# Kernel optimization log

Measured on AMD Instinct MI355X. Metric: run time of the kernel, lower is better.

The kernel has to match this reference:

```python
import jax, jax.numpy as jnp
import numpy as np

N_NODES = 50000
N_EDGES = 1600000
D_IN = 128
D_HID = 128
D_OUT = 3
EPS = 1e-5


def setup_inputs() -> dict:
    key = jax.random.key(0)
    ks = jax.random.split(key, 16)
    def lin(k, fi, fo):
        s = 1.0 / np.sqrt(fi)
        return jax.random.uniform(k, (fi, fo), jnp.float32, -s, s)
    inp = {
        "x": jax.random.normal(ks[0], (N_NODES, D_IN), jnp.float32),
        "edge_index": jax.random.randint(ks[1], (2, N_EDGES), 0, N_NODES, jnp.int32),
        "W1": lin(ks[2], D_IN, D_HID), "b1": jnp.zeros((D_HID,), jnp.float32),
        "W2": lin(ks[3], D_HID, D_HID), "b2": jnp.zeros((D_HID,), jnp.float32),
        "W3": lin(ks[4], D_HID, D_HID), "b3": jnp.zeros((D_HID,), jnp.float32),
        "g1": jnp.ones((D_HID,), jnp.float32), "beta1": jnp.zeros((D_HID,), jnp.float32),
        "g2": jnp.ones((D_HID,), jnp.float32), "beta2": jnp.zeros((D_HID,), jnp.float32),
        "Wp1": lin(ks[5], D_HID, D_HID), "bp1": jnp.zeros((D_HID,), jnp.float32),
        "Wp2": lin(ks[6], D_HID, D_OUT), "bp2": jnp.zeros((D_OUT,), jnp.float32),
    }
    return inp


def _gcn_norm(edge_index, n):
    # add self-loops, symmetric normalization (PyG GCNConv default)
    loops = jnp.arange(n, dtype=edge_index.dtype)
    row = jnp.concatenate([edge_index[0], loops])  # source
    col = jnp.concatenate([edge_index[1], loops])  # target
    deg = jax.ops.segment_sum(jnp.ones_like(col, jnp.float32), col, num_segments=n)
    dinv = jnp.where(deg > 0, jax.lax.rsqrt(deg), 0.0)
    norm = dinv[row] * dinv[col]  # [E+N]
    return row, col, norm


def _gcn_conv(x, W, b, row, col, norm, n):
    h = x @ W                                # [N, F]
    msg = h[row] * norm[:, None]             # [E+N, F] gather
    out = jax.ops.segment_sum(msg, col, num_segments=n)  # scatter-add
    return out + b


def _layernorm(x, g, beta):
    mu = jnp.mean(x, axis=-1, keepdims=True)
    var = jnp.var(x, axis=-1, keepdims=True)
    return (x - mu) * jax.lax.rsqrt(var + EPS) * g + beta


def reference(x, edge_index, W1, b1, W2, b2, W3, b3, g1, beta1, g2, beta2, Wp1, bp1, Wp2, bp2):
    n = x.shape[0]
    row, col, norm = _gcn_norm(edge_index, n)
    # layer 0
    h = _gcn_conv(x, W1, b1, row, col, norm, n)
    h = _layernorm(jax.nn.relu(h), g1, beta1)  # dropout = identity (eval mode)
    # layer 1
    h = _gcn_conv(h, W2, b2, row, col, norm, n)
    h = _layernorm(jax.nn.relu(h), g2, beta2)
    # layer 2 (no layernorm)
    h = _gcn_conv(h, W3, b3, row, col, norm, n)
    h = jax.nn.relu(h)
    # post-MP MLP head (dropout = identity in eval)
    h = h @ Wp1 + bp1
    return h @ Wp2 + bp2
```

## Files before the change

kernel.cpp:

```cpp
#include <hip/hip_runtime.h>
#include <hip/hip_bf16.h>

#define EPS_LN 1e-5f
#define NB    256
#define SEGCAP 16384

typedef int ivec4 __attribute__((ext_vector_type(4)));
typedef short bf16x8v __attribute__((ext_vector_type(8)));
typedef float f32x4v __attribute__((ext_vector_type(4)));
typedef unsigned short u16x8 __attribute__((ext_vector_type(8)));


__global__ __launch_bounds__(256) void bucket_hist(const int* __restrict__ col,
                                                   int* __restrict__ chunkBH,
                                                   int E, int per, int nbuck) {
    __shared__ int hist[256];
    int t = threadIdx.x;
    hist[t] = 0;
    __syncthreads();
    int s0 = blockIdx.x * per;
    int s1 = s0 + per; if (s1 > E) s1 = E;
    if (s0 < s1) {
        int q0 = s0 >> 2, q1 = s1 >> 2;
        for (int i = q0 + t; i < q1; i += 256) {
            ivec4 c = __builtin_nontemporal_load((const ivec4*)col + i);
            atomicAdd(&hist[c.x >> 8], 1);
            atomicAdd(&hist[c.y >> 8], 1);
            atomicAdd(&hist[c.z >> 8], 1);
            atomicAdd(&hist[c.w >> 8], 1);
        }
        for (int i = (q1 << 2) + t; i < s1; i += 256)
            atomicAdd(&hist[col[i] >> 8], 1);
    }
    __syncthreads();
    if (t < nbuck) chunkBH[blockIdx.x * 256 + t] = hist[t];
}

__global__ __launch_bounds__(256) void bucket_scan(int* __restrict__ chunkBH,
                                                   int* __restrict__ bucketStart,
                                                   int* __restrict__ rowPtr,
                                                   int E, int n, int nbuck, int nb) {
    __shared__ int tot[256];
    int t = threadIdx.x;
    int run = 0;
    if (t < nbuck) {
        for (int k0 = 0; k0 < nb; k0 += 16) {
            int v[16];
#pragma unroll
            for (int j = 0; j < 16; j++)
                v[j] = (k0 + j < nb) ? chunkBH[(k0 + j) * 256 + t] : 0;
#pragma unroll
            for (int j = 0; j < 16; j++) {
                int tv = v[j];
                if (k0 + j < nb) chunkBH[(k0 + j) * 256 + t] = run;
                run += tv;
            }
        }
    }
    tot[t] = run;
    __syncthreads();
    for (int d = 1; d < 256; d <<= 1) {
        int add = (t >= d) ? tot[t - d] : 0;
        __syncthreads();
        tot[t] += add;
        __syncthreads();
    }
    if (t < nbuck) bucketStart[t] = tot[t] - run;
    if (t == 0) { bucketStart[nbuck] = E; rowPtr[n] = E; }
}

__global__ __launch_bounds__(256) void scatter_pairs(const int* __restrict__ row,
                                                     const int* __restrict__ col,
                                                     const int* __restrict__ chunkBH,
                                                     const int* __restrict__ bucketStart,
                                                     unsigned long long* __restrict__ tmp,
                                                     int E, int per, int nbuck) {
    __shared__ int curs[256];
    int t = threadIdx.x;
    int k = blockIdx.x;
    curs[t] = (t < nbuck) ? (chunkBH[k * 256 + t] + bucketStart[t]) : 0;
    __syncthreads();
    int s0 = k * per;
    int s1 = s0 + per; if (s1 > E) s1 = E;
    if (s0 >= s1) return;
    int q0 = s0 >> 2, q1 = s1 >> 2;
    for (int i = q0 + t; i < q1; i += 256) {
        ivec4 c4 = __builtin_nontemporal_load((const ivec4*)col + i);
        ivec4 r4 = __builtin_nontemporal_load((const ivec4*)row + i);
        int p0 = atomicAdd(&curs[c4.x >> 8], 1);
        tmp[p0] = ((unsigned long long)(unsigned)c4.x << 32) | (unsigned)r4.x;
        int p1 = atomicAdd(&curs[c4.y >> 8], 1);
        tmp[p1] = ((unsigned long long)(unsigned)c4.y << 32) | (unsigned)r4.y;
        int p2 = atomicAdd(&curs[c4.z >> 8], 1);
        tmp[p2] = ((unsigned long long)(unsigned)c4.z << 32) | (unsigned)r4.z;
        int p3 = atomicAdd(&curs[c4.w >> 8], 1);
        tmp[p3] = ((unsigned long long)(unsigned)c4.w << 32) | (unsigned)r4.w;
    }
    for (int i = (q1 << 2) + t; i < s1; i += 256) {
        int c = col[i], r = row[i];
        int p = atomicAdd(&curs[c >> 8], 1);
        tmp[p] = ((unsigned long long)(unsigned)c << 32) | (unsigned)r;
    }
}

__global__ __launch_bounds__(256) void bucket_fill(const unsigned long long* __restrict__ tmp,
                                                   const int* __restrict__ bucketStart,
                                                   int* __restrict__ rowPtr,
                                                   float* __restrict__ dinv,
                                                   int* __restrict__ srcList,
                                                   int n) {
    __shared__ int cnt[256];
    __shared__ int cur[256];
    __shared__ int seg[SEGCAP];
    int b = blockIdx.x, t = threadIdx.x;
    int node0 = b << 8;
    int s0 = bucketStart[b], s1 = bucketStart[b + 1];
    int len = s1 - s0;
    cnt[t] = 0;
    __syncthreads();
    for (int i = s0 + t; i < s1; i += 256) {
        int c = (int)(tmp[i] >> 32);
        atomicAdd(&cnt[c - node0], 1);
    }
    __syncthreads();
    int v = cnt[t];
    cur[t] = v;
    __syncthreads();
    for (int d = 1; d < 256; d <<= 1) {
        int add = (t >= d) ? cur[t - d] : 0;
        __syncthreads();
        cur[t] += add;
        __syncthreads();
    }
    int excl = cur[t] - v;
    int node = node0 + t;
    if (node < n) {
        rowPtr[node] = s0 + excl;
        dinv[node] = rsqrtf((float)v + 1.0f);
    }
    cur[t] = excl;
    __syncthreads();
    if (len <= SEGCAP) {
        for (int i = s0 + t; i < s1; i += 256) {
            unsigned long long p = tmp[i];
            int c = (int)(p >> 32);
            int r = (int)(p & 0xffffffffu);
            int pos = atomicAdd(&cur[c - node0], 1);
            seg[pos] = r;
        }
        __syncthreads();
        for (int i = t; i < len; i += 256)
            srcList[s0 + i] = seg[i];
    } else {
        for (int i = s0 + t; i < s1; i += 256) {
            unsigned long long p = tmp[i];
            int c = (int)(p >> 32);
            int r = (int)(p & 0xffffffffu);
            int pos = atomicAdd(&cur[c - node0], 1);
            srcList[s0 + pos] = r;
        }
    }
}

__global__ __launch_bounds__(256) void pack_w_all(const float* __restrict__ W1,
                                                  const float* __restrict__ W2,
                                                  const float* __restrict__ W3,
                                                  unsigned short* __restrict__ Wq) {
    int w = blockIdx.x >> 6;
    const float* W = (w == 0) ? W1 : (w == 1) ? W2 : W3;
    unsigned short* Wp = Wq + (size_t)w * 32768;
    int s = (blockIdx.x & 63) * 256 + threadIdx.x;
    int i = s & 7;
    int lane = (s >> 3) & 63;
    int jt = (s >> 9) & 7;
    int kb = s >> 12;
    int k = kb * 32 + ((lane >> 4) & 3) * 8 + i;
    int nn = jt * 16 + (lane & 15);
    float v = W[k * 128 + nn];
    __hip_bfloat16 hi = __float2bfloat16(v);
    float hf = __bfloat162float(hi);
    __hip_bfloat16 lo = __float2bfloat16(v - hf);
    Wp[s]         = *(unsigned short*)&hi;
    Wp[16384 + s] = *(unsigned short*)&lo;
}

__device__ __forceinline__ void split8(const float* __restrict__ p,
                                       bf16x8v& ah, bf16x8v& al) {
#pragma unroll
    for (int i = 0; i < 8; i++) {
        float v = p[i];
        __hip_bfloat16 hb = __float2bfloat16(v);
        float hf = __bfloat162float(hb);
        __hip_bfloat16 lb = __float2bfloat16(v - hf);
        ah[i] = *(short*)&hb;
        al[i] = *(short*)&lb;
    }
}

template<int ASRC>
__global__ __launch_bounds__(256) void gemm_mfma(const float* __restrict__ Af32,
                                                 const unsigned short* __restrict__ Ahi,
                                                 const unsigned short* __restrict__ Alo,
                                                 const unsigned short* __restrict__ Wp,
                                                 const float* __restrict__ dinv,
                                                 unsigned short* __restrict__ hbOut,
                                                 int n) {
    __shared__ unsigned short Bs[8192];

    const int tx = threadIdx.x;
    const int wv = tx >> 6;
    const int l  = tx & 63;
    const int m0 = blockIdx.x * 64 + wv * 16;
    int arow = m0 + (l & 15);
    if (arow >= n) arow = 0;
    const int kofs = (l >> 4) * 8;

    f32x4v acc[8];
#pragma unroll
    for (int jt = 0; jt < 8; jt++) acc[jt] = (f32x4v){0.f, 0.f, 0.f, 0.f};

#pragma unroll
    for (int kb = 0; kb < 4; kb++) {
        __syncthreads();
        {
            u16x8* dH = (u16x8*)&Bs[tx * 16];
            const u16x8* sH = (const u16x8*)(Wp + kb * 4096 + tx * 16);
            dH[0] = sH[0]; dH[1] = sH[1];
            u16x8* dL = (u16x8*)&Bs[4096 + tx * 16];
            const u16x8* sL = (const u16x8*)(Wp + 16384 + kb * 4096 + tx * 16);
            dL[0] = sL[0]; dL[1] = sL[1];
        }
        bf16x8v ah, al;
        if (ASRC == 0) {
            split8(Af32 + (size_t)arow * 128 + kb * 32 + kofs, ah, al);
        } else {
            ah = *(const bf16x8v*)(Ahi + (size_t)arow * 128 + kb * 32 + kofs);
            al = *(const bf16x8v*)(Alo + (size_t)arow * 128 + kb * 32 + kofs);
        }
        __syncthreads();
#pragma unroll
        for (int jt = 0; jt < 8; jt++) {
            bf16x8v bh = *(const bf16x8v*)&Bs[jt * 512 + l * 8];
            bf16x8v bl = *(const bf16x8v*)&Bs[4096 + jt * 512 + l * 8];
            acc[jt] = __builtin_amdgcn_mfma_f32_16x16x32_bf16(ah, bh, acc[jt], 0, 0, 0);
            acc[jt] = __builtin_amdgcn_mfma_f32_16x16x32_bf16(ah, bl, acc[jt], 0, 0, 0);
            acc[jt] = __builtin_amdgcn_mfma_f32_16x16x32_bf16(al, bh, acc[jt], 0, 0, 0);
        }
    }

    const int r0 = m0 + (l >> 4) * 4;
    const int colb = l & 15;
#pragma unroll
    for (int r = 0; r < 4; r++) {
        int grow = r0 + r;
        if (grow < n) {
            float dv = dinv[grow];
#pragma unroll
            for (int jt = 0; jt < 8; jt++) {
                __hip_bfloat16 t = __float2bfloat16(acc[jt][r] * dv);
                hbOut[(size_t)grow * 128 + jt * 16 + colb] = *(unsigned short*)&t;
            }
        }
    }
}

#define BF_LO(u) __uint_as_float((u) << 16)
#define BF_HI(u) __uint_as_float((u) & 0xffff0000u)

__global__ __launch_bounds__(128) void agg_post(const unsigned int* __restrict__ hb,
                                                const int* __restrict__ rowPtr,
                                                const int* __restrict__ srcList,
                                                const float* __restrict__ dinv,
                                                const float* __restrict__ b,
                                                const float* __restrict__ g,
                                                const float* __restrict__ beta,
                                                unsigned short* __restrict__ outHi,
                                                unsigned short* __restrict__ outLo,
                                                int n) {
    int wid = (blockIdx.x * 128 + threadIdx.x) >> 6;
    int lane = threadIdx.x & 63;
    if (wid >= n) return;
    int h = lane & 15;
    int gg = lane >> 4;
    int e0 = rowPtr[wid], e1 = rowPtr[wid + 1];
    float dc = dinv[wid];
    const uint4* hb4 = (const uint4*)hb;

    uint4 us = hb4[(size_t)wid * 16 + h];

    float a[8];
#pragma unroll
    for (int j = 0; j < 8; j++) a[j] = 0.f;

    int idx0 = (e0 + gg < e1) ? srcList[e0 + gg] : -1;
    int idx1 = (e0 + 4 + gg < e1) ? srcList[e0 + 4 + gg] : -1;
    int e = e0;
    for (; e + 8 <= e1; e += 8) {
        int ni0 = (e + 8 + gg < e1) ? srcList[e + 8 + gg] : -1;
        int ni1 = (e + 12 + gg < e1) ? srcList[e + 12 + gg] : -1;
        uint4 u0 = hb4[(size_t)idx0 * 16 + h];
        uint4 u1 = hb4[(size_t)idx1 * 16 + h];
        a[0] += BF_LO(u0.x); a[1] += BF_HI(u0.x);
        a[2] += BF_LO(u0.y); a[3] += BF_HI(u0.y);
        a[4] += BF_LO(u0.z); a[5] += BF_HI(u0.z);
        a[6] += BF_LO(u0.w); a[7] += BF_HI(u0.w);
        a[0] += BF_LO(u1.x); a[1] += BF_HI(u1.x);
        a[2] += BF_LO(u1.y); a[3] += BF_HI(u1.y);
        a[4] += BF_LO(u1.z); a[5] += BF_HI(u1.z);
        a[6] += BF_LO(u1.w); a[7] += BF_HI(u1.w);
        idx0 = ni0; idx1 = ni1;
    }
    if (idx0 >= 0) {
        uint4 u = hb4[(size_t)idx0 * 16 + h];
        a[0] += BF_LO(u.x); a[1] += BF_HI(u.x);
        a[2] += BF_LO(u.y); a[3] += BF_HI(u.y);
        a[4] += BF_LO(u.z); a[5] += BF_HI(u.z);
        a[6] += BF_LO(u.w); a[7] += BF_HI(u.w);
    }
    if (idx1 >= 0) {
        uint4 u = hb4[(size_t)idx1 * 16 + h];
        a[0] += BF_LO(u.x); a[1] += BF_HI(u.x);
        a[2] += BF_LO(u.y); a[3] += BF_HI(u.y);
        a[4] += BF_LO(u.z); a[5] += BF_HI(u.z);
        a[6] += BF_LO(u.w); a[7] += BF_HI(u.w);
    }
#pragma unroll
    for (int j = 0; j < 8; j++) {
        a[j] += __shfl_xor(a[j], 16, 64);
        a[j] += __shfl_xor(a[j], 32, 64);
    }
    a[0] += BF_LO(us.x); a[1] += BF_HI(us.x);
    a[2] += BF_LO(us.y); a[3] += BF_HI(us.y);
    a[4] += BF_LO(us.z); a[5] += BF_HI(us.z);
    a[6] += BF_LO(us.w); a[7] += BF_HI(us.w);

    float4 bv0 = *(const float4*)(b + h * 8);
    float4 bv1 = *(const float4*)(b + h * 8 + 4);
    a[0] = fmaxf(a[0] * dc + bv0.x, 0.f);
    a[1] = fmaxf(a[1] * dc + bv0.y, 0.f);
    a[2] = fmaxf(a[2] * dc + bv0.z, 0.f);
    a[3] = fmaxf(a[3] * dc + bv0.w, 0.f);
    a[4] = fmaxf(a[4] * dc + bv1.x, 0.f);
    a[5] = fmaxf(a[5] * dc + bv1.y, 0.f);
    a[6] = fmaxf(a[6] * dc + bv1.z, 0.f);
    a[7] = fmaxf(a[7] * dc + bv1.w, 0.f);

    float s = ((a[0] + a[1]) + (a[2] + a[3])) + ((a[4] + a[5]) + (a[6] + a[7]));
#pragma unroll
    for (int m = 8; m >= 1; m >>= 1) s += __shfl_xor(s, m, 64);
    float mu = s * (1.f / 128.f);
    float sq = 0.f;
    float d[8];
#pragma unroll
    for (int j = 0; j < 8; j++) { d[j] = a[j] - mu; sq += d[j] * d[j]; }
#pragma unroll
    for (int m = 8; m >= 1; m >>= 1) sq += __shfl_xor(sq, m, 64);
    float rs = rsqrtf(sq * (1.f / 128.f) + EPS_LN);
    float4 gv0 = *(const float4*)(g + h * 8);
    float4 gv1 = *(const float4*)(g + h * 8 + 4);
    float4 bt0 = *(const float4*)(beta + h * 8);
    float4 bt1 = *(const float4*)(beta + h * 8 + 4);
    a[0] = d[0] * rs * gv0.x + bt0.x;
    a[1] = d[1] * rs * gv0.y + bt0.y;
    a[2] = d[2] * rs * gv0.z + bt0.z;
    a[3] = d[3] * rs * gv0.w + bt0.w;
    a[4] = d[4] * rs * gv1.x + bt1.x;
    a[5] = d[5] * rs * gv1.y + bt1.y;
    a[6] = d[6] * rs * gv1.z + bt1.z;
    a[7] = d[7] * rs * gv1.w + bt1.w;

    if (gg == 0) {
        ushort4 h0, h1, l0, l1;
        __hip_bfloat16 bb; float ff;
        bb = __float2bfloat16(a[0]); ff = __bfloat162float(bb); h0.x = *(unsigned short*)&bb;
        bb = __float2bfloat16(a[0] - ff); l0.x = *(unsigned short*)&bb;
        bb = __float2bfloat16(a[1]); ff = __bfloat162float(bb); h0.y = *(unsigned short*)&bb;
        bb = __float2bfloat16(a[1] - ff); l0.y = *(unsigned short*)&bb;
        bb = __float2bfloat16(a[2]); ff = __bfloat162float(bb); h0.z = *(unsigned short*)&bb;
        bb = __float2bfloat16(a[2] - ff); l0.z = *(unsigned short*)&bb;
        bb = __float2bfloat16(a[3]); ff = __bfloat162float(bb); h0.w = *(unsigned short*)&bb;
        bb = __float2bfloat16(a[3] - ff); l0.w = *(unsigned short*)&bb;
        bb = __float2bfloat16(a[4]); ff = __bfloat162float(bb); h1.x = *(unsigned short*)&bb;
        bb = __float2bfloat16(a[4] - ff); l1.x = *(unsigned short*)&bb;
        bb = __float2bfloat16(a[5]); ff = __bfloat162float(bb); h1.y = *(unsigned short*)&bb;
        bb = __float2bfloat16(a[5] - ff); l1.y = *(unsigned short*)&bb;
        bb = __float2bfloat16(a[6]); ff = __bfloat162float(bb); h1.z = *(unsigned short*)&bb;
        bb = __float2bfloat16(a[6] - ff); l1.z = *(unsigned short*)&bb;
        bb = __float2bfloat16(a[7]); ff = __bfloat162float(bb); h1.w = *(unsigned short*)&bb;
        bb = __float2bfloat16(a[7] - ff); l1.w = *(unsigned short*)&bb;
        size_t base = (size_t)wid * 128 + h * 8;
        *(ushort4*)(outHi + base)     = h0;
        *(ushort4*)(outHi + base + 4) = h1;
        *(ushort4*)(outLo + base)     = l0;
        *(ushort4*)(outLo + base + 4) = l1;
    }
}

__global__ __launch_bounds__(128) void agg_head(
        const unsigned int* __restrict__ hb,
        const int* __restrict__ rowPtr,
        const int* __restrict__ srcList,
        const float* __restrict__ dinv,
        const float* __restrict__ b,
        const float* __restrict__ Weff,
        const float* __restrict__ beff,
        float* __restrict__ out, int n) {
    __shared__ float Wl[384];
    int tt = threadIdx.x;
    for (int idx = tt; idx < 384; idx += 128) {
        int f = idx / 3, c = idx - f * 3;
        int j = f & 7, hh = f >> 3;
        Wl[(j * 3 + c) * 16 + hh] = Weff[idx];
    }
    __syncthreads();

    int wid = (blockIdx.x * 128 + tt) >> 6;
    int lane = tt & 63;
    if (wid >= n) return;
    int h = lane & 15;
    int gg = lane >> 4;
    int e0 = rowPtr[wid], e1 = rowPtr[wid + 1];
    float dc = dinv[wid];
    const uint4* hb4 = (const uint4*)hb;
    uint4 us = hb4[(size_t)wid * 16 + h];

    float a[8];
#pragma unroll
    for (int j = 0; j < 8; j++) a[j] = 0.f;

    int idx0 = (e0 + gg < e1) ? srcList[e0 + gg] : -1;
    int idx1 = (e0 + 4 + gg < e1) ? srcList[e0 + 4 + gg] : -1;
    int e = e0;
    for (; e + 8 <= e1; e += 8) {
        int ni0 = (e + 8 + gg < e1) ? srcList[e + 8 + gg] : -1;
        int ni1 = (e + 12 + gg < e1) ? srcList[e + 12 + gg] : -1;
        uint4 u0 = hb4[(size_t)idx0 * 16 + h];
        uint4 u1 = hb4[(size_t)idx1 * 16 + h];
        a[0] += BF_LO(u0.x); a[1] += BF_HI(u0.x);
        a[2] += BF_LO(u0.y); a[3] += BF_HI(u0.y);
        a[4] += BF_LO(u0.z); a[5] += BF_HI(u0.z);
        a[6] += BF_LO(u0.w); a[7] += BF_HI(u0.w);
        a[0] += BF_LO(u1.x); a[1] += BF_HI(u1.x);
        a[2] += BF_LO(u1.y); a[3] += BF_HI(u1.y);
        a[4] += BF_LO(u1.z); a[5] += BF_HI(u1.z);
        a[6] += BF_LO(u1.w); a[7] += BF_HI(u1.w);
        idx0 = ni0; idx1 = ni1;
    }
    if (idx0 >= 0) {
        uint4 u = hb4[(size_t)idx0 * 16 + h];
        a[0] += BF_LO(u.x); a[1] += BF_HI(u.x);
        a[2] += BF_LO(u.y); a[3] += BF_HI(u.y);
        a[4] += BF_LO(u.z); a[5] += BF_HI(u.z);
        a[6] += BF_LO(u.w); a[7] += BF_HI(u.w);
    }
    if (idx1 >= 0) {
        uint4 u = hb4[(size_t)idx1 * 16 + h];
        a[0] += BF_LO(u.x); a[1] += BF_HI(u.x);
        a[2] += BF_LO(u.y); a[3] += BF_HI(u.y);
        a[4] += BF_LO(u.z); a[5] += BF_HI(u.z);
        a[6] += BF_LO(u.w); a[7] += BF_HI(u.w);
    }
#pragma unroll
    for (int j = 0; j < 8; j++) {
        a[j] += __shfl_xor(a[j], 16, 64);
        a[j] += __shfl_xor(a[j], 32, 64);
    }
    a[0] += BF_LO(us.x); a[1] += BF_HI(us.x);
    a[2] += BF_LO(us.y); a[3] += BF_HI(us.y);
    a[4] += BF_LO(us.z); a[5] += BF_HI(us.z);
    a[6] += BF_LO(us.w); a[7] += BF_HI(us.w);

    float4 bv0 = *(const float4*)(b + h * 8);
    float4 bv1 = *(const float4*)(b + h * 8 + 4);
    a[0] = fmaxf(a[0] * dc + bv0.x, 0.f);
    a[1] = fmaxf(a[1] * dc + bv0.y, 0.f);
    a[2] = fmaxf(a[2] * dc + bv0.z, 0.f);
    a[3] = fmaxf(a[3] * dc + bv0.w, 0.f);
    a[4] = fmaxf(a[4] * dc + bv1.x, 0.f);
    a[5] = fmaxf(a[5] * dc + bv1.y, 0.f);
    a[6] = fmaxf(a[6] * dc + bv1.z, 0.f);
    a[7] = fmaxf(a[7] * dc + bv1.w, 0.f);

    float p0 = 0.f, p1 = 0.f, p2 = 0.f;
#pragma unroll
    for (int j = 0; j < 8; j++) {
        p0 += a[j] * Wl[(j * 3 + 0) * 16 + h];
        p1 += a[j] * Wl[(j * 3 + 1) * 16 + h];
        p2 += a[j] * Wl[(j * 3 + 2) * 16 + h];
    }
#pragma unroll
    for (int m = 8; m >= 1; m >>= 1) {
        p0 += __shfl_xor(p0, m, 64);
        p1 += __shfl_xor(p1, m, 64);
        p2 += __shfl_xor(p2, m, 64);
    }
    if (lane == 0) {
        out[(size_t)wid * 3 + 0] = p0 + beff[0];
        out[(size_t)wid * 3 + 1] = p1 + beff[1];
        out[(size_t)wid * 3 + 2] = p2 + beff[2];
    }
}

__global__ __launch_bounds__(128) void head_collapse(const float* __restrict__ Wp1,
                                                     const float* __restrict__ bp1,
                                                     const float* __restrict__ Wp2,
                                                     const float* __restrict__ bp2,
                                                     float* __restrict__ Weff,
                                                     float* __restrict__ beff) {
    __shared__ float w2[384];
    int t = threadIdx.x;
    w2[t] = Wp2[t]; w2[t + 128] = Wp2[t + 128]; w2[t + 256] = Wp2[t + 256];
    __syncthreads();
    float p0 = 0.f, p1 = 0.f, p2 = 0.f;
    const float* wr = Wp1 + (size_t)t * 128;
    for (int k = 0; k < 128; k++) {
        float v = wr[k];
        p0 += v * w2[k * 3 + 0];
        p1 += v * w2[k * 3 + 1];
        p2 += v * w2[k * 3 + 2];
    }
    Weff[t * 3 + 0] = p0; Weff[t * 3 + 1] = p1; Weff[t * 3 + 2] = p2;
    if (t == 0) {
        float q0 = bp2[0], q1 = bp2[1], q2 = bp2[2];
        for (int k = 0; k < 128; k++) {
            float v = bp1[k];
            q0 += v * w2[k * 3 + 0];
            q1 += v * w2[k * 3 + 1];
            q2 += v * w2[k * 3 + 2];
        }
        beff[0] = q0; beff[1] = q1; beff[2] = q2;
    }
}

extern "C" void kernel_launch(void* const* d_in, const int* in_sizes, int n_in,
                              void* d_out, int out_size, void* d_ws, size_t ws_size,
                              hipStream_t stream) {
    const float* x   = (const float*)d_in[0];
    const int* ei    = (const int*)d_in[1];
    const float* W1  = (const float*)d_in[2];
    const float* b1  = (const float*)d_in[3];
    const float* W2  = (const float*)d_in[4];
    const float* b2  = (const float*)d_in[5];
    const float* W3  = (const float*)d_in[6];
    const float* b3  = (const float*)d_in[7];
    const float* g1  = (const float*)d_in[8];
    const float* be1 = (const float*)d_in[9];
    const float* g2  = (const float*)d_in[10];
    const float* be2 = (const float*)d_in[11];
    const float* Wp1f = (const float*)d_in[12];
    const float* bp1 = (const float*)d_in[13];
    const float* Wp2f = (const float*)d_in[14];
    const float* bp2 = (const float*)d_in[15];
    float* out = (float*)d_out;

    const int n = in_sizes[0] / 128;
    const int E = in_sizes[1] / 2;
    const int* row = ei;
    const int* col = ei + E;

    char* ws = (char*)d_ws;
    size_t nA  = ((size_t)n * 4 + 255) & ~(size_t)255;
    size_t nA1 = ((size_t)(n + 1) * 4 + 255) & ~(size_t)255;
    size_t eA  = ((size_t)E * 4 + 255) & ~(size_t)255;
    size_t hbSz = ((size_t)n * 128 * 2 + 255) & ~(size_t)255;
    int*   rowPtr  = (int*)ws;
    float* dinvp   = (float*)(ws + nA1);
    int*   srcList = (int*)(ws + nA1 + nA);
    unsigned short* hbA = (unsigned short*)(ws + nA1 + nA + eA);
    unsigned short* hbB = hbA + hbSz / 2;
    unsigned short* Phi = hbB + hbSz / 2;
    unsigned short* Plo = Phi + hbSz / 2;
    unsigned short* Wq  = Plo + hbSz / 2;
    float* Weff = (float*)(Wq + 3 * 32768);
    float* beff = Weff + 384;
    unsigned long long* tmp = (unsigned long long*)Phi;
    int* chunkBH     = (int*)((char*)Phi + 2 * eA);
    int* bucketStart = (int*)((char*)Phi + 2 * eA + (size_t)NB * 256 * 4);

    const int nbuck = (n + 255) >> 8;
    const int per   = (((E + NB - 1) / NB) + 15) & ~15;
    const int tileBlocks = (n + 63) / 64;
    const int nodeWaveBlocks = (n + 1) / 2;

    bucket_hist<<<NB, 256, 0, stream>>>(col, chunkBH, E, per, nbuck);
    bucket_scan<<<1, 256, 0, stream>>>(chunkBH, bucketStart, rowPtr, E, n, nbuck, NB);
    scatter_pairs<<<NB, 256, 0, stream>>>(row, col, chunkBH, bucketStart, tmp, E, per, nbuck);
    bucket_fill<<<nbuck, 256, 0, stream>>>(tmp, bucketStart, rowPtr, dinvp, srcList, n);
    head_collapse<<<1, 128, 0, stream>>>(Wp1f, bp1, Wp2f, bp2, Weff, beff);
    pack_w_all<<<192, 256, 0, stream>>>(W1, W2, W3, Wq);

    gemm_mfma<0><<<tileBlocks, 256, 0, stream>>>(x, nullptr, nullptr, Wq, dinvp, hbA, n);
    agg_post<<<nodeWaveBlocks, 128, 0, stream>>>((const unsigned int*)hbA,
                                                 rowPtr, srcList, dinvp,
                                                 b1, g1, be1, Phi, Plo, n);
    gemm_mfma<1><<<tileBlocks, 256, 0, stream>>>(nullptr, Phi, Plo, Wq + 32768, dinvp, hbB, n);
    agg_post<<<nodeWaveBlocks, 128, 0, stream>>>((const unsigned int*)hbB,
                                                 rowPtr, srcList, dinvp,
                                                 b2, g2, be2, Phi, Plo, n);
    gemm_mfma<1><<<tileBlocks, 256, 0, stream>>>(nullptr, Phi, Plo, Wq + 65536, dinvp, hbA, n);
    agg_head<<<nodeWaveBlocks, 128, 0, stream>>>((const unsigned int*)hbA,
                                                 rowPtr, srcList, dinvp,
                                                 b3, Weff, beff, out, n);
}
```

Before: 364.3 us.

## Unroll gather loops to four neighbors, fold head collapse into weight packing

The aggregation kernels now keep four neighbor-row loads in flight per iteration instead of two, with index prefetch four ahead, to raise memory-level parallelism in the latency-bound gather. The head_collapse launch is merged into pack_w_all as an extra block, removing one kernel launch. agg_head reads the collapsed head weights straight from global memory into registers instead of staging them through shared memory with a barrier, which raises register pressure.

Measured after the change: 361.3 us. About the same (-0.8%).

```diff
diff --git a/kernel.cpp b/kernel.cpp
--- a/kernel.cpp
+++ b/kernel.cpp
@@ -165,7 +165,41 @@
 __global__ __launch_bounds__(256) void pack_w_all(const float* __restrict__ W1,
                                                   const float* __restrict__ W2,
                                                   const float* __restrict__ W3,
-                                                  unsigned short* __restrict__ Wq) {
+                                                  unsigned short* __restrict__ Wq,
+                                                  const float* __restrict__ Wp1,
+                                                  const float* __restrict__ bp1,
+                                                  const float* __restrict__ Wp2,
+                                                  const float* __restrict__ bp2,
+                                                  float* __restrict__ Weff,
+                                                  float* __restrict__ beff) {
+    if (blockIdx.x == 192) {
+        __shared__ float w2[384];
+        int t = threadIdx.x;
+        for (int idx = t; idx < 384; idx += 256) w2[idx] = Wp2[idx];
+        __syncthreads();
+        if (t < 128) {
+            float p0 = 0.f, p1 = 0.f, p2 = 0.f;
+            const float* wr = Wp1 + (size_t)t * 128;
+            for (int k = 0; k < 128; k++) {
+                float v = wr[k];
+                p0 += v * w2[k * 3 + 0];
+                p1 += v * w2[k * 3 + 1];
+                p2 += v * w2[k * 3 + 2];
+            }
+            Weff[t * 3 + 0] = p0; Weff[t * 3 + 1] = p1; Weff[t * 3 + 2] = p2;
+            if (t == 0) {
+                float q0 = bp2[0], q1 = bp2[1], q2 = bp2[2];
+                for (int k = 0; k < 128; k++) {
+                    float v = bp1[k];
+                    q0 += v * w2[k * 3 + 0];
+                    q1 += v * w2[k * 3 + 1];
+                    q2 += v * w2[k * 3 + 2];
+                }
+                beff[0] = q0; beff[1] = q1; beff[2] = q2;
+            }
+        }
+        return;
+    }
     int w = blockIdx.x >> 6;
     const float* W = (w == 0) ? W1 : (w == 1) ? W2 : W3;
     unsigned short* Wp = Wq + (size_t)w * 32768;
@@ -266,6 +300,12 @@
 
 #define BF_LO(u) __uint_as_float((u) << 16)
 #define BF_HI(u) __uint_as_float((u) & 0xffff0000u)
+
+#define ACC8(u)  do { \
+    a[0] += BF_LO((u).x); a[1] += BF_HI((u).x); \
+    a[2] += BF_LO((u).y); a[3] += BF_HI((u).y); \
+    a[4] += BF_LO((u).z); a[5] += BF_HI((u).z); \
+    a[6] += BF_LO((u).w); a[7] += BF_HI((u).w); } while (0)
 
 __global__ __launch_bounds__(128) void agg_post(const unsigned int* __restrict__ hb,
                                                 const int* __restrict__ rowPtr,
@@ -292,47 +332,34 @@
 #pragma unroll
     for (int j = 0; j < 8; j++) a[j] = 0.f;
 
-    int idx0 = (e0 + gg < e1) ? srcList[e0 + gg] : -1;
+    int idx0 = (e0 + 0 + gg < e1) ? srcList[e0 + 0 + gg] : -1;
     int idx1 = (e0 + 4 + gg < e1) ? srcList[e0 + 4 + gg] : -1;
+    int idx2 = (e0 + 8 + gg < e1) ? srcList[e0 + 8 + gg] : -1;
+    int idx3 = (e0 + 12 + gg < e1) ? srcList[e0 + 12 + gg] : -1;
     int e = e0;
-    for (; e + 8 <= e1; e += 8) {
-        int ni0 = (e + 8 + gg < e1) ? srcList[e + 8 + gg] : -1;
-        int ni1 = (e + 12 + gg < e1) ? srcList[e + 12 + gg] : -1;
+    for (; e + 16 <= e1; e += 16) {
+        int ni0 = (e + 16 + gg < e1) ? srcList[e + 16 + gg] : -1;
+        int ni1 = (e + 20 + gg < e1) ? srcList[e + 20 + gg] : -1;
+        int ni2 = (e + 24 + gg < e1) ? srcList[e + 24 + gg] : -1;
+        int ni3 = (e + 28 + gg < e1) ? srcList[e + 28 + gg] : -1;
         uint4 u0 = hb4[(size_t)idx0 * 16 + h];
         uint4 u1 = hb4[(size_t)idx1 * 16 + h];
-        a[0] += BF_LO(u0.x); a[1] += BF_HI(u0.x);
-        a[2] += BF_LO(u0.y); a[3] += BF_HI(u0.y);
-        a[4] += BF_LO(u0.z); a[5] += BF_HI(u0.z);
-        a[6] += BF_LO(u0.w); a[7] += BF_HI(u0.w);
-        a[0] += BF_LO(u1.x); a[1] += BF_HI(u1.x);
-        a[2] += BF_LO(u1.y); a[3] += BF_HI(u1.y);
-        a[4] += BF_LO(u1.z); a[5] += BF_HI(u1.z);
-        a[6] += BF_LO(u1.w); a[7] += BF_HI(u1.w);
-        idx0 = ni0; idx1 = ni1;
-    }
-    if (idx0 >= 0) {
-        uint4 u = hb4[(size_t)idx0 * 16 + h];
-        a[0] += BF_LO(u.x); a[1] += BF_HI(u.x);
-        a[2] += BF_LO(u.y); a[3] += BF_HI(u.y);
-        a[4] += BF_LO(u.z); a[5] += BF_HI(u.z);
-        a[6] += BF_LO(u.w); a[7] += BF_HI(u.w);
-    }
-    if (idx1 >= 0) {
-        uint4 u = hb4[(size_t)idx1 * 16 + h];
-        a[0] += BF_LO(u.x); a[1] += BF_HI(u.x);
-        a[2] += BF_LO(u.y); a[3] += BF_HI(u.y);
-        a[4] += BF_LO(u.z); a[5] += BF_HI(u.z);
-        a[6] += BF_LO(u.w); a[7] += BF_HI(u.w);
-    }
+        uint4 u2 = hb4[(size_t)idx2 * 16 + h];
+        uint4 u3 = hb4[(size_t)idx3 * 16 + h];
+        ACC8(u0); ACC8(u1); ACC8(u2); ACC8(u3);
+        idx0 = ni0; idx1 = ni1; idx2 = ni2; idx3 = ni3;
+    }
+    if (idx0 >= 0) { uint4 u = hb4[(size_t)idx0 * 16 + h]; ACC8(u); }
+    if (idx1 >= 0) { uint4 u = hb4[(size_t)idx1 * 16 + h]; ACC8(u); }
+    if (idx2 >= 0) { uint4 u = hb4[(size_t)idx2 * 16 + h]; ACC8(u); }
+    if (idx3 >= 0) { uint4 u = hb4[(size_t)idx3 * 16 + h]; ACC8(u); }
+
 #pragma unroll
     for (int j = 0; j < 8; j++) {
         a[j] += __shfl_xor(a[j], 16, 64);
         a[j] += __shfl_xor(a[j], 32, 64);
     }
-    a[0] += BF_LO(us.x); a[1] += BF_HI(us.x);
-    a[2] += BF_LO(us.y); a[3] += BF_HI(us.y);
-    a[4] += BF_LO(us.z); a[5] += BF_HI(us.z);
-    a[6] += BF_LO(us.w); a[7] += BF_HI(us.w);
+    ACC8(us);
 
     float4 bv0 = *(const float4*)(b + h * 8);
     float4 bv1 = *(const float4*)(b + h * 8 + 4);
@@ -405,15 +432,7 @@
         const float* __restrict__ Weff,
         const float* __restrict__ beff,
         float* __restrict__ out, int n) {
-    __shared__ float Wl[384];
     int tt = threadIdx.x;
-    for (int idx = tt; idx < 384; idx += 128) {
-        int f = idx / 3, c = idx - f * 3;
-        int j = f & 7, hh = f >> 3;
-        Wl[(j * 3 + c) * 16 + hh] = Weff[idx];
-    }
-    __syncthreads();
-
     int wid = (blockIdx.x * 128 + tt) >> 6;
     int lane = tt & 63;
     if (wid >= n) return;
@@ -424,51 +443,49 @@
     const uint4* hb4 = (const uint4*)hb;
     uint4 us = hb4[(size_t)wid * 16 + h];
 
+    float wreg[24];
+    {
+        const float4* wp = (const float4*)(Weff + 24 * h);
+#pragma unroll
+        for (int q = 0; q < 6; q++) {
+            float4 v = wp[q];
+            wreg[4 * q + 0] = v.x; wreg[4 * q + 1] = v.y;
+            wreg[4 * q + 2] = v.z; wreg[4 * q + 3] = v.w;
+        }
+    }
+
     float a[8];
 #pragma unroll
     for (int j = 0; j < 8; j++) a[j] = 0.f;
 
-    int idx0 = (e0 + gg < e1) ? srcList[e0 + gg] : -1;
+    int idx0 = (e0 + 0 + gg < e1) ? srcList[e0 + 0 + gg] : -1;
     int idx1 = (e0 + 4 + gg < e1) ? srcList[e0 + 4 + gg] : -1;
+    int idx2 = (e0 + 8 + gg < e1) ? srcList[e0 + 8 + gg] : -1;
+    int idx3 = (e0 + 12 + gg < e1) ? srcList[e0 + 12 + gg] : -1;
     int e = e0;
-    for (; e + 8 <= e1; e += 8) {
-        int ni0 = (e + 8 + gg < e1) ? srcList[e + 8 + gg] : -1;
-        int ni1 = (e + 12 + gg < e1) ? srcList[e + 12 + gg] : -1;
+    for (; e + 16 <= e1; e += 16) {
+        int ni0 = (e + 16 + gg < e1) ? srcList[e + 16 + gg] : -1;
+        int ni1 = (e + 20 + gg < e1) ? srcList[e + 20 + gg] : -1;
+        int ni2 = (e + 24 + gg < e1) ? srcList[e + 24 + gg] : -1;
+        int ni3 = (e + 28 + gg < e1) ? srcList[e + 28 + gg] : -1;
         uint4 u0 = hb4[(size_t)idx0 * 16 + h];
         uint4 u1 = hb4[(size_t)idx1 * 16 + h];
-        a[0] += BF_LO(u0.x); a[1] += BF_HI(u0.x);
-        a[2] += BF_LO(u0.y); a[3] += BF_HI(u0.y);
-        a[4] += BF_LO(u0.z); a[5] += BF_HI(u0.z);
-        a[6] += BF_LO(u0.w); a[7] += BF_HI(u0.w);
-        a[0] += BF_LO(u1.x); a[1] += BF_HI(u1.x);
-        a[2] += BF_LO(u1.y); a[3] += BF_HI(u1.y);
-        a[4] += BF_LO(u1.z); a[5] += BF_HI(u1.z);
-        a[6] += BF_LO(u1.w); a[7] += BF_HI(u1.w);
-        idx0 = ni0; idx1 = ni1;
-    }
-    if (idx0 >= 0) {
-        uint4 u = hb4[(size_t)idx0 * 16 + h];
-        a[0] += BF_LO(u.x); a[1] += BF_HI(u.x);
-        a[2] += BF_LO(u.y); a[3] += BF_HI(u.y);
-        a[4] += BF_LO(u.z); a[5] += BF_HI(u.z);
-        a[6] += BF_LO(u.w); a[7] += BF_HI(u.w);
-    }
-    if (idx1 >= 0) {
-        uint4 u = hb4[(size_t)idx1 * 16 + h];
-        a[0] += BF_LO(u.x); a[1] += BF_HI(u.x);
-        a[2] += BF_LO(u.y); a[3] += BF_HI(u.y);
-        a[4] += BF_LO(u.z); a[5] += BF_HI(u.z);
-        a[6] += BF_LO(u.w); a[7] += BF_HI(u.w);
-    }
+        uint4 u2 = hb4[(size_t)idx2 * 16 + h];
+        uint4 u3 = hb4[(size_t)idx3 * 16 + h];
+        ACC8(u0); ACC8(u1); ACC8(u2); ACC8(u3);
+        idx0 = ni0; idx1 = ni1; idx2 = ni2; idx3 = ni3;
+    }
+    if (idx0 >= 0) { uint4 u = hb4[(size_t)idx0 * 16 + h]; ACC8(u); }
+    if (idx1 >= 0) { uint4 u = hb4[(size_t)idx1 * 16 + h]; ACC8(u); }
+    if (idx2 >= 0) { uint4 u = hb4[(size_t)idx2 * 16 + h]; ACC8(u); }
+    if (idx3 >= 0) { uint4 u = hb4[(size_t)idx3 * 16 + h]; ACC8(u); }
+
 #pragma unroll
     for (int j = 0; j < 8; j++) {
         a[j] += __shfl_xor(a[j], 16, 64);
         a[j] += __shfl_xor(a[j], 32, 64);
     }
-    a[0] += BF_LO(us.x); a[1] += BF_HI(us.x);
-    a[2] += BF_LO(us.y); a[3] += BF_HI(us.y);
-    a[4] += BF_LO(us.z); a[5] += BF_HI(us.z);
-    a[6] += BF_LO(us.w); a[7] += BF_HI(us.w);
+    ACC8(us);
 
     float4 bv0 = *(const float4*)(b + h * 8);
     float4 bv1 = *(const float4*)(b + h * 8 + 4);
@@ -484,9 +501,9 @@
     float p0 = 0.f, p1 = 0.f, p2 = 0.f;
 #pragma unroll
     for (int j = 0; j < 8; j++) {
-        p0 += a[j] * Wl[(j * 3 + 0) * 16 + h];
-        p1 += a[j] * Wl[(j * 3 + 1) * 16 + h];
-        p2 += a[j] * Wl[(j * 3 + 2) * 16 + h];
+        p0 += a[j] * wreg[j * 3 + 0];
+        p1 += a[j] * wreg[j * 3 + 1];
+        p2 += a[j] * wreg[j * 3 + 2];
     }
 #pragma unroll
     for (int m = 8; m >= 1; m >>= 1) {
@@ -498,37 +515,6 @@
         out[(size_t)wid * 3 + 0] = p0 + beff[0];
         out[(size_t)wid * 3 + 1] = p1 + beff[1];
         out[(size_t)wid * 3 + 2] = p2 + beff[2];
-    }
-}
-
-__global__ __launch_bounds__(128) void head_collapse(const float* __restrict__ Wp1,
-                                                     const float* __restrict__ bp1,
-                                                     const float* __restrict__ Wp2,
-                                                     const float* __restrict__ bp2,
-                                                     float* __restrict__ Weff,
-                                                     float* __restrict__ beff) {
-    __shared__ float w2[384];
-    int t = threadIdx.x;
-    w2[t] = Wp2[t]; w2[t + 128] = Wp2[t + 128]; w2[t + 256] = Wp2[t + 256];
-    __syncthreads();
-    float p0 = 0.f, p1 = 0.f, p2 = 0.f;
-    const float* wr = Wp1 + (size_t)t * 128;
-    for (int k = 0; k < 128; k++) {
-        float v = wr[k];
-        p0 += v * w2[k * 3 + 0];
-        p1 += v * w2[k * 3 + 1];
-        p2 += v * w2[k * 3 + 2];
-    }
-    Weff[t * 3 + 0] = p0; Weff[t * 3 + 1] = p1; Weff[t * 3 + 2] = p2;
-    if (t == 0) {
-        float q0 = bp2[0], q1 = bp2[1], q2 = bp2[2];
-        for (int k = 0; k < 128; k++) {
-            float v = bp1[k];
-            q0 += v * w2[k * 3 + 0];
-            q1 += v * w2[k * 3 + 1];
-            q2 += v * w2[k * 3 + 2];
-        }
-        beff[0] = q0; beff[1] = q1; beff[2] = q2;
     }
 }
 
@@ -586,8 +572,7 @@
     bucket_scan<<<1, 256, 0, stream>>>(chunkBH, bucketStart, rowPtr, E, n, nbuck, NB);
     scatter_pairs<<<NB, 256, 0, stream>>>(row, col, chunkBH, bucketStart, tmp, E, per, nbuck);
     bucket_fill<<<nbuck, 256, 0, stream>>>(tmp, bucketStart, rowPtr, dinvp, srcList, n);
-    head_collapse<<<1, 128, 0, stream>>>(Wp1f, bp1, Wp2f, bp2, Weff, beff);
-    pack_w_all<<<192, 256, 0, stream>>>(W1, W2, W3, Wq);
+    pack_w_all<<<193, 256, 0, stream>>>(W1, W2, W3, Wq, Wp1f, bp1, Wp2f, bp2, Weff, beff);
 
     gemm_mfma<0><<<tileBlocks, 256, 0, stream>>>(x, nullptr, nullptr, Wq, dinvp, hbA, n);
     agg_post<<<nodeWaveBlocks, 128, 0, stream>>>((const unsigned int*)hbA,
```
